# Optimization experiments

Measured on AMD Instinct MI355X. Metric: run time of the kernel, lower is better.

Reference implementation:

```python
import jax, jax.numpy as jnp
import numpy as np

U = 356  # LSTM units

def _lstm(x, W, Wr, b, h0, c0):
    """Keras-style LSTM. x: [B,T,F]. Returns (hs [B,T,U], h [B,U], c [B,U])."""
    def step(carry, xt):
        h, c = carry
        z = xt @ W + h @ Wr + b            # [B, 4U], gate order i,f,g,o
        i, f, g, o = jnp.split(z, 4, axis=-1)
        c = jax.nn.sigmoid(f) * c + jax.nn.sigmoid(i) * jnp.tanh(g)
        h = jax.nn.sigmoid(o) * jnp.tanh(c)
        return (h, c), h
    (h, c), hs = jax.lax.scan(step, (h0, c0), jnp.swapaxes(x, 0, 1))
    return jnp.swapaxes(hs, 0, 1), h, c


def setup_inputs() -> dict:
    key = jax.random.key(0)
    ks = jax.random.split(key, 12)
    s = 0.05
    return {
        "x": jax.random.normal(ks[0], (8192, 7, 69), jnp.float32),
        "m": jax.random.normal(ks[1], (8192, 7, 45), jnp.float32),
        "enc_W": jax.random.normal(ks[2], (69, 4 * U), jnp.float32) * s,
        "enc_U": jax.random.normal(ks[3], (U, 4 * U), jnp.float32) * s,
        "enc_b": jnp.zeros((4 * U,), jnp.float32),
        "dec_W": jax.random.normal(ks[4], (45, 4 * U), jnp.float32) * s,
        "dec_U": jax.random.normal(ks[5], (U, 4 * U), jnp.float32) * s,
        "dec_b": jnp.zeros((4 * U,), jnp.float32),
        "W_map": jax.random.normal(ks[6], (7 * U, 1024), jnp.float32) * s,
        "b_map": jnp.zeros((1024,), jnp.float32),
        "W1": jax.random.normal(ks[7], (1024, 1024), jnp.float32) * s,
        "b1": jnp.zeros((1024,), jnp.float32),
        "W2": jax.random.normal(ks[8], (1024, 1024), jnp.float32) * s,
        "b2": jnp.zeros((1024,), jnp.float32),
        "W3": jax.random.normal(ks[9], (1024, 1024), jnp.float32) * s,
        "b3": jnp.zeros((1024,), jnp.float32),
        "W_out": jax.random.normal(ks[10], (1024, 168), jnp.float32) * s,
        "b_out": jnp.zeros((168,), jnp.float32),
    }


def reference(x, m, enc_W, enc_U, enc_b, dec_W, dec_U, dec_b,
              W_map, b_map, W1, b1, W2, b2, W3, b3, W_out, b_out):
    B = x.shape[0]
    h0 = jnp.zeros((B, U), x.dtype)
    c0 = jnp.zeros((B, U), x.dtype)
    # Encoder: only final states are used (dropout layers are identity at inference).
    _, s_h, s_c = _lstm(x, enc_W, enc_U, enc_b, h0, c0)
    # Decoder seeded with encoder states, returns full sequence [B,7,U].
    decoded, _, _ = _lstm(m, dec_W, dec_U, dec_b, s_h, s_c)
    f = decoded.reshape(B, -1)                     # [B, 7*356]
    h = jax.nn.relu(f @ W_map + b_map)
    h = jnp.tanh(h @ W1 + b1)
    h = jnp.tanh(h @ W2 + b2)
    h = jnp.tanh(h @ W3 + b3)
    return h @ W_out + b_out                        # [B, 168]
```

## Files before the change

kernel.cpp:

```cpp
#include <hip/hip_runtime.h>
#include <math.h>


using bf16x8 = __attribute__((ext_vector_type(8))) short;
using f32x4  = __attribute__((ext_vector_type(4))) float;

enum { EPI_NONE = 0, EPI_RELU = 1, EPI_TANH = 2 };

__device__ inline unsigned short f2bf(float f) {
    union { float f; unsigned u; } v; v.f = f;
    unsigned r = v.u + 0x7FFFu + ((v.u >> 16) & 1u);
    return (unsigned short)(r >> 16);
}
__device__ inline float sigf(float x) {
    return __fdividef(1.f, 1.f + __expf(-x));
}
__device__ inline float tanhfast(float x) {
    return 1.f - __fdividef(2.f, 1.f + __expf(2.f * x));
}

__device__ inline void gll16(const void* g, void* l) {
    __builtin_amdgcn_global_load_lds(
        (const __attribute__((address_space(1))) unsigned int*)(uintptr_t)g,
        (__attribute__((address_space(3))) unsigned int*)(unsigned int)(uintptr_t)l,
        16, 0, 0);
}

#define PROWS 32
#define PLDA  456

#define STAGE_CHUNK(bufv, kkv, partv)                                          \
    _Pragma("unroll")                                                          \
    for (int q = 0; q < 4; ++q)                                                \
        gll16(Wt + (size_t)(kkv) * 49152 + (w * 12 + (partv) * 4 + q) * 512    \
                  + lane * 8,                                                  \
              (void*)&Bs[((w * 3 + (bufv)) * 4 + q) * 512 + lane * 8]);

#define LOADB4(dst, bufv)                                                      \
    _Pragma("unroll")                                                          \
    for (int q = 0; q < 4; ++q)                                                \
        dst[q] = *(const bf16x8*)&Bs[((w * 3 + (bufv)) * 4 + q) * 512          \
                                     + lane * 8];

#define LOADA(dst, kkv)                                                        \
    _Pragma("unroll")                                                          \
    for (int mi = 0; mi < 2; ++mi)                                             \
        dst[mi] = *(const bf16x8*)&Ab[(mi * 16 + lm) * PLDA + (kkv) * 32       \
                                      + quad * 8];

#define MFMA8(partv, bRv)                                                      \
    _Pragma("unroll")                                                          \
    for (int q = 0; q < 4; ++q) {                                              \
        acc[0][(partv) * 4 + q] = __builtin_amdgcn_mfma_f32_16x16x32_bf16(     \
            aF[0], bRv[q], acc[0][(partv) * 4 + q], 0, 0, 0);                  \
        acc[1][(partv) * 4 + q] = __builtin_amdgcn_mfma_f32_16x16x32_bf16(     \
            aF[1], bRv[q], acc[1][(partv) * 4 + q], 0, 0, 0);                  \
    }

#define VMWAIT(n)                                                              \
    asm volatile("s_waitcnt vmcnt(" #n ")" ::: "memory");                      \
    __builtin_amdgcn_sched_barrier(0);

__global__ __attribute__((amdgpu_flat_work_group_size(512, 512),
                          amdgpu_waves_per_eu(2, 2)))
void lstm_persist(const float* __restrict__ x,
                  const float* __restrict__ m,
                  const unsigned short* __restrict__ WtE,
                  const unsigned short* __restrict__ WtD,
                  const float* __restrict__ bIE,
                  const float* __restrict__ bID,
                  unsigned short* __restrict__ dcd)
{
    __shared__ __attribute__((aligned(16))) unsigned short Ab[PROWS * PLDA];
    __shared__ __attribute__((aligned(16))) unsigned short Bs[49152];
    const int tid  = threadIdx.x;
    const int lane = tid & 63;
    const int w    = tid >> 6;
    const int lm   = lane & 15, quad = lane >> 4;
    const int brow = blockIdx.x * PROWS;
    const int kk0  = blockIdx.x % 14;

    for (int i = tid; i < PROWS * PLDA; i += 512) Ab[i] = 0;
    __syncthreads();
    for (int i = tid; i < PROWS * 69; i += 512) {
        const int r = i / 69, f = i - r * 69;
        Ab[r * PLDA + f] = f2bf(x[((size_t)(brow + r) * 7 + 0) * 69 + f]);
    }

    float creg[2][3][4] = {};
    float bI[3][4];

    for (int s = 0; s < 14; ++s) {
        const bool enc = (s < 7);
        const int t = enc ? s : s - 7;
        const unsigned short* Wt = enc ? WtE : WtD;

        if (s == 0 || s == 7) {
            const float* bsrc = enc ? bIE : bID;
            #pragma unroll
            for (int a = 0; a < 3; ++a)
                #pragma unroll
                for (int g = 0; g < 4; ++g)
                    bI[a][g] = bsrc[(3 * w + a) * 64 + g * 16 + lm];
        }

        __syncthreads();

        f32x4 acc[2][12] = {};
        {
            STAGE_CHUNK(0, kk0, 0)
            STAGE_CHUNK(1, kk0, 1)
            int kkc = kk0;
            #pragma unroll 1
            for (int i = 0; i < 14; ++i) {
                const int kkn = (kkc == 13) ? 0 : kkc + 1;
                bf16x8 aF[2], bR[4];
                STAGE_CHUNK(2, kkc, 2)
                VMWAIT(8)
                LOADA(aF, kkc)
                LOADB4(bR, 0)
                MFMA8(0, bR)
                if (i < 13) {
                    STAGE_CHUNK(0, kkn, 0)
                    VMWAIT(8)
                } else {
                    VMWAIT(4)
                }
                LOADB4(bR, 1)
                MFMA8(1, bR)
                if (i < 13) {
                    STAGE_CHUNK(1, kkn, 1)
                    VMWAIT(8)
                } else {
                    VMWAIT(0)
                }
                LOADB4(bR, 2)
                MFMA8(2, bR)
                kkc = kkn;
            }
        }

        __syncthreads();

        const int hoff = (s < 6) ? 69 : 45;
        #pragma unroll
        for (int mi = 0; mi < 2; ++mi)
            #pragma unroll
            for (int a = 0; a < 3; ++a) {
                const int u = (3 * w + a) * 16 + lm;
                const bool uok = (u < 356);
                #pragma unroll
                for (int r = 0; r < 4; ++r) {
                    const float zi = acc[mi][a * 4 + 0][r] + bI[a][0];
                    const float zf = acc[mi][a * 4 + 1][r] + bI[a][1];
                    const float zg = acc[mi][a * 4 + 2][r] + bI[a][2];
                    const float zo = acc[mi][a * 4 + 3][r] + bI[a][3];
                    const float cn = sigf(zf) * creg[mi][a][r]
                                   + sigf(zi) * tanhfast(zg);
                    creg[mi][a][r] = cn;
                    const unsigned short hb = f2bf(sigf(zo) * tanhfast(cn));
                    const int rl = mi * 16 + quad * 4 + r;
                    if (uok) {
                        if (s < 13) Ab[rl * PLDA + hoff + u] = hb;
                        if (!enc)
                            dcd[(size_t)(brow + rl) * 2496 + t * 356 + u] = hb;
                    }
                }
            }

        const int sn = s + 1;
        if (sn < 7) {
            for (int i = tid; i < PROWS * 69; i += 512) {
                const int r = i / 69, f = i - r * 69;
                Ab[r * PLDA + f] =
                    f2bf(x[((size_t)(brow + r) * 7 + sn) * 69 + f]);
            }
        } else if (sn < 14) {
            for (int i = tid; i < PROWS * 45; i += 512) {
                const int r = i / 45, f = i - r * 45;
                Ab[r * PLDA + f] =
                    f2bf(m[((size_t)(brow + r) * 7 + (sn - 7)) * 45 + f]);
            }
        }
    }
}


#define STAGE(A_, Bt_, K_, k0_, b_)                                            \
    {                                                                          \
        const int row = tid >> 2, kc = tid & 3;                                \
        gll16((A_)  + (size_t)(m0 + row) * (K_) + (k0_) + kc * 8,              \
              (void*)&As[b_][tid * 8]);                                        \
        gll16((Bt_) + (size_t)(n0 + row) * (K_) + (k0_) + kc * 8,              \
              (void*)&Bs[b_][tid * 8]);                                        \
    }

#define GEMM_CORE(A_, Bt_, K_)                                                 \
    STAGE(A_, Bt_, K_, 0, 0)                                                   \
    {                                                                          \
        const int niter = (K_) / 32;                                           \
        for (int it = 0; it < niter; ++it) {                                   \
            __syncthreads();                                                   \
            if (it + 1 < niter) {                                              \
                const int kn = (it + 1) * 32, bn = (it + 1) & 1;               \
                STAGE(A_, Bt_, K_, kn, bn)                                     \
            }                                                                  \
            const unsigned short* Asb = As[it & 1];                            \
            const unsigned short* Bsb = Bs[it & 1];                            \
            bf16x8 aF[2], bF[4];                                               \
            _Pragma("unroll")                                                  \
            for (int mi = 0; mi < 2; ++mi)                                     \
                aF[mi] = *(const bf16x8*)(Asb + (wr*32 + mi*16 + lm)*32 + quad*8);\
            _Pragma("unroll")                                                  \
            for (int ni = 0; ni < 4; ++ni)                                     \
                bF[ni] = *(const bf16x8*)(Bsb + (wc*64 + ni*16 + lm)*32 + quad*8);\
            _Pragma("unroll")                                                  \
            for (int mi = 0; mi < 2; ++mi)                                     \
                _Pragma("unroll")                                              \
                for (int ni = 0; ni < 4; ++ni)                                 \
                    acc[mi][ni] = __builtin_amdgcn_mfma_f32_16x16x32_bf16(     \
                        aF[mi], bF[ni], acc[mi][ni], 0, 0, 0);                 \
        }                                                                      \
    }

#define GEMM_PREAMBLE                                                          \
    __shared__ __attribute__((aligned(16))) unsigned short As[2][128 * 32];    \
    __shared__ __attribute__((aligned(16))) unsigned short Bs[2][128 * 32];    \
    const int tid  = threadIdx.x;                                              \
    const int lane = tid & 63;                                                 \
    const int w    = tid >> 6;                                       \
    const int wr   = w >> 1, wc = w & 1;                    \
    const int lm   = lane & 15, quad = lane >> 4;                              \
    const int m0   = blockIdx.x * 128, n0 = blockIdx.y * 128;                  \
    f32x4 acc[2][4] = {};

template <int EPI, int OUT_BF16, int NGUARD>
__global__ __launch_bounds__(512, 6)
void gemm_mfma(const unsigned short* __restrict__ A,
               const unsigned short* __restrict__ Bt,
               const float* __restrict__ bias,
               void* __restrict__ Cv, int ldc, int Nreal, int K)
{
    GEMM_PREAMBLE
    GEMM_CORE(A, Bt, K)
    #pragma unroll
    for (int mi = 0; mi < 2; ++mi)
        #pragma unroll
        for (int r = 0; r < 4; ++r) {
            const size_t row = m0 + wr * 32 + mi * 16 + quad * 4 + r;
            #pragma unroll
            for (int ni = 0; ni < 4; ++ni) {
                const int col = n0 + wc * 64 + ni * 16 + lm;
                if (!NGUARD || col < Nreal) {
                    float v = acc[mi][ni][r] + bias[col];
                    if (EPI == EPI_RELU) v = fmaxf(v, 0.f);
                    if (EPI == EPI_TANH) v = tanhfast(v);
                    if (OUT_BF16) ((unsigned short*)Cv)[row * ldc + col] = f2bf(v);
                    else          ((float*)Cv)[row * ldc + col] = v;
                }
            }
        }
}

struct PackArgs {
    const float *Wa0, *Wb0, *bias0; unsigned short* Wt0; float* bI0; int K10, K0, Kp0;
    const float *Wa1, *Wb1, *bias1; unsigned short* Wt1; float* bI1; int K11, K1, Kp1;
};
__global__ void pack_lstm2(PackArgs p)
{
    const float* Wa  = blockIdx.y ? p.Wa1  : p.Wa0;
    const float* Wb  = blockIdx.y ? p.Wb1  : p.Wb0;
    const float* bias= blockIdx.y ? p.bias1: p.bias0;
    unsigned short* Wt = blockIdx.y ? p.Wt1 : p.Wt0;
    float* biasI = blockIdx.y ? p.bI1 : p.bI0;
    const int K1 = blockIdx.y ? p.K11 : p.K10;
    const int K  = blockIdx.y ? p.K1  : p.K0;
    const int Kp = blockIdx.y ? p.Kp1 : p.Kp0;
    const int idx = blockIdx.x * 256 + threadIdx.x;
    if (idx >= 1536 * Kp) return;
    const int np = idx / Kp, k = idx - np * Kp;
    const int ub = np >> 6, g = (np >> 4) & 3, ul = np & 15;
    const int u = ub * 16 + ul;
    const bool valid = (u < 356);
    const int norig = g * 356 + u;
    float v = 0.f;
    if (valid && k < K)
        v = (k < K1) ? Wa[(size_t)k * 1424 + norig]
                     : Wb[(size_t)(k - K1) * 1424 + norig];
    const int wv = np / 192, rem = np - wv * 192;
    const int ni = rem >> 4, lmv = rem & 15;
    const int kkv = k >> 5, kq = k & 31;
    const int qd = kq >> 3, j = kq & 7;
    Wt[(size_t)kkv * 49152 + (size_t)(wv * 12 + ni) * 512 + (qd * 16 + lmv) * 8 + j]
        = f2bf(v);
    if (k == 0) biasI[np] = valid ? bias[norig] : 0.f;
}

__global__ void transpose_pack(const float* __restrict__ W, int K, int N,
                               unsigned short* __restrict__ Wt, int Kp, int Np)
{
    __shared__ float t[32][33];
    const int n0 = blockIdx.x * 32, k0 = blockIdx.y * 32;
    const int tx = threadIdx.x, ty = threadIdx.y;
    #pragma unroll
    for (int r = 0; r < 4; ++r) {
        const int k = k0 + ty + 8 * r, n = n0 + tx;
        t[ty + 8 * r][tx] = (k < K && n < N) ? W[(size_t)k * N + n] : 0.f;
    }
    __syncthreads();
    #pragma unroll
    for (int r = 0; r < 4; ++r) {
        const int k = k0 + tx, n = n0 + ty + 8 * r;
        if (k < Kp && n < Np) Wt[(size_t)n * Kp + k] = f2bf(t[tx][ty + 8 * r]);
    }
}

struct WP3 { const float *s0, *s1, *s2; unsigned short *d0, *d1, *d2; };
__global__ void transpose_pack3(WP3 p)
{
    __shared__ float t[32][33];
    const float* W = (blockIdx.z == 0) ? p.s0 : (blockIdx.z == 1) ? p.s1 : p.s2;
    unsigned short* Wt = (blockIdx.z == 0) ? p.d0 : (blockIdx.z == 1) ? p.d1 : p.d2;
    const int n0 = blockIdx.x * 32, k0 = blockIdx.y * 32;
    const int tx = threadIdx.x, ty = threadIdx.y;
    #pragma unroll
    for (int r = 0; r < 4; ++r)
        t[ty + 8 * r][tx] = W[(size_t)(k0 + ty + 8 * r) * 1024 + n0 + tx];
    __syncthreads();
    #pragma unroll
    for (int r = 0; r < 4; ++r)
        Wt[(size_t)(n0 + ty + 8 * r) * 1024 + k0 + tx] = f2bf(t[tx][ty + 8 * r]);
}

__global__ void zero_dcd_pad(unsigned short* __restrict__ dcd)
{
    const int i = blockIdx.x * 256 + threadIdx.x;
    if (i < 8192 * 4) dcd[(size_t)(i >> 2) * 2496 + 2492 + (i & 3)] = 0;
}

extern "C" void kernel_launch(void* const* d_in, const int* in_sizes, int n_in,
                              void* d_out, int out_size, void* d_ws, size_t ws_size,
                              hipStream_t stream)
{
    const float* x     = (const float*)d_in[0];
    const float* m     = (const float*)d_in[1];
    const float* enc_W = (const float*)d_in[2];
    const float* enc_U = (const float*)d_in[3];
    const float* enc_b = (const float*)d_in[4];
    const float* dec_W = (const float*)d_in[5];
    const float* dec_Um= (const float*)d_in[6];
    const float* dec_b = (const float*)d_in[7];
    const float* W_map = (const float*)d_in[8];
    const float* b_map = (const float*)d_in[9];
    const float* W1    = (const float*)d_in[10];
    const float* b1    = (const float*)d_in[11];
    const float* W2    = (const float*)d_in[12];
    const float* b2    = (const float*)d_in[13];
    const float* W3    = (const float*)d_in[14];
    const float* b3    = (const float*)d_in[15];
    const float* W_out = (const float*)d_in[16];
    const float* b_out = (const float*)d_in[17];
    float* out = (float*)d_out;

    const int B = 8192, FE = 69, FD = 45;
    const int KMP = 2496;

    char* ws = (char*)d_ws;
    size_t off = 0;
    auto alloc = [&](size_t bytes) -> void* {
        void* p = ws + off; off = (off + bytes + 255) & ~(size_t)255; return p;
    };
    unsigned short* WtE = (unsigned short*)alloc((size_t)1536 * 448 * 2);
    unsigned short* WtD = (unsigned short*)alloc((size_t)1536 * 448 * 2);
    unsigned short* WtM = (unsigned short*)alloc((size_t)1024 * KMP * 2);
    unsigned short* Wt1 = (unsigned short*)alloc((size_t)1024 * 1024 * 2);
    unsigned short* Wt2 = (unsigned short*)alloc((size_t)1024 * 1024 * 2);
    unsigned short* Wt3 = (unsigned short*)alloc((size_t)1024 * 1024 * 2);
    unsigned short* WtO = (unsigned short*)alloc((size_t)256 * 1024 * 2);
    float* bIE = (float*)alloc(1536 * 4);
    float* bID = (float*)alloc(1536 * 4);
    unsigned short* dcd = (unsigned short*)alloc((size_t)B * KMP * 2);
    unsigned short* a1  = (unsigned short*)alloc((size_t)B * 1024 * 2);
    unsigned short* a2  = (unsigned short*)alloc((size_t)B * 1024 * 2);

    PackArgs pa{enc_W, enc_U, enc_b, WtE, bIE, FE, FE + 356, 448,
                dec_W, dec_Um, dec_b, WtD, bID, FD, FD + 356, 448};
    pack_lstm2<<<dim3((1536 * 448 + 255) / 256, 2), 256, 0, stream>>>(pa);
    const dim3 tb(32, 8);
    transpose_pack<<<dim3(1024 / 32, KMP / 32), tb, 0, stream>>>(
        W_map, 2492, 1024, WtM, KMP, 1024);
    WP3 p3{W1, W2, W3, Wt1, Wt2, Wt3};
    transpose_pack3<<<dim3(32, 32, 3), tb, 0, stream>>>(p3);
    transpose_pack<<<dim3(256 / 32, 1024 / 32), tb, 0, stream>>>(
        W_out, 1024, 168, WtO, 1024, 256);
    zero_dcd_pad<<<(8192 * 4 + 255) / 256, 256, 0, stream>>>(dcd);

    lstm_persist<<<256, 512, 0, stream>>>(x, m, WtE, WtD, bIE, bID, dcd);

    gemm_mfma<EPI_RELU, 1, 0><<<dim3(64, 8), 512, 0, stream>>>(
        dcd, WtM, b_map, a1, 1024, 1024, KMP);
    gemm_mfma<EPI_TANH, 1, 0><<<dim3(64, 8), 512, 0, stream>>>(
        a1, Wt1, b1, a2, 1024, 1024, 1024);
    gemm_mfma<EPI_TANH, 1, 0><<<dim3(64, 8), 512, 0, stream>>>(
        a2, Wt2, b2, a1, 1024, 1024, 1024);
    gemm_mfma<EPI_TANH, 1, 0><<<dim3(64, 8), 512, 0, stream>>>(
        a1, Wt3, b3, a2, 1024, 1024, 1024);
    gemm_mfma<EPI_NONE, 0, 1><<<dim3(64, 2), 512, 0, stream>>>(
        a2, WtO, b_out, out, 168, 168, 1024);
}
```

Baseline: 570.2 us.

## Split LSTM gate columns across 12 waves instead of 8 in persistent kernel

The persistent LSTM kernel now launches 768 threads per block (12 waves), and each wave owns 2 unit groups (8 gate tiles) instead of 3 (12 tiles). The weight staging pipeline shrinks from three chunk buffers per wave to two, with adjusted vmcnt waits, and the accumulator and cell-state register arrays get smaller. The aim is more waves sharing the recurrent GEMM per block, with less register pressure per wave, which should improve latency hiding. In exchange each wave issues fewer MFMAs between waits, so the shallower double-buffer may expose more load latency. The waves_per_eu hint is also removed.

```diff
diff --git a/kernel.cpp b/kernel.cpp
--- a/kernel.cpp
+++ b/kernel.cpp
@@ -32,14 +32,14 @@
 #define STAGE_CHUNK(bufv, kkv, partv)                                          \
     _Pragma("unroll")                                                          \
     for (int q = 0; q < 4; ++q)                                                \
-        gll16(Wt + (size_t)(kkv) * 49152 + (w * 12 + (partv) * 4 + q) * 512    \
+        gll16(Wt + (size_t)(kkv) * 49152 + (w * 8 + (partv) * 4 + q) * 512     \
                   + lane * 8,                                                  \
-              (void*)&Bs[((w * 3 + (bufv)) * 4 + q) * 512 + lane * 8]);
+              (void*)&Bs[((w * 2 + (bufv)) * 4 + q) * 512 + lane * 8]);
 
 #define LOADB4(dst, bufv)                                                      \
     _Pragma("unroll")                                                          \
     for (int q = 0; q < 4; ++q)                                                \
-        dst[q] = *(const bf16x8*)&Bs[((w * 3 + (bufv)) * 4 + q) * 512          \
+        dst[q] = *(const bf16x8*)&Bs[((w * 2 + (bufv)) * 4 + q) * 512          \
                                      + lane * 8];
 
 #define LOADA(dst, kkv)                                                        \
@@ -61,8 +61,7 @@
     asm volatile("s_waitcnt vmcnt(" #n ")" ::: "memory");                      \
     __builtin_amdgcn_sched_barrier(0);
 
-__global__ __attribute__((amdgpu_flat_work_group_size(512, 512),
-                          amdgpu_waves_per_eu(2, 2)))
+__global__ __attribute__((amdgpu_flat_work_group_size(768, 768)))
 void lstm_persist(const float* __restrict__ x,
                   const float* __restrict__ m,
                   const unsigned short* __restrict__ WtE,
@@ -80,15 +79,15 @@
     const int brow = blockIdx.x * PROWS;
     const int kk0  = blockIdx.x % 14;
 
-    for (int i = tid; i < PROWS * PLDA; i += 512) Ab[i] = 0;
+    for (int i = tid; i < PROWS * PLDA; i += 768) Ab[i] = 0;
     __syncthreads();
-    for (int i = tid; i < PROWS * 69; i += 512) {
+    for (int i = tid; i < PROWS * 69; i += 768) {
         const int r = i / 69, f = i - r * 69;
         Ab[r * PLDA + f] = f2bf(x[((size_t)(brow + r) * 7 + 0) * 69 + f]);
     }
 
-    float creg[2][3][4] = {};
-    float bI[3][4];
+    float creg[2][2][4] = {};
+    float bI[2][4];
 
     for (int s = 0; s < 14; ++s) {
         const bool enc = (s < 7);
@@ -98,15 +97,15 @@
         if (s == 0 || s == 7) {
             const float* bsrc = enc ? bIE : bID;
             #pragma unroll
-            for (int a = 0; a < 3; ++a)
+            for (int uu = 0; uu < 2; ++uu)
                 #pragma unroll
                 for (int g = 0; g < 4; ++g)
-                    bI[a][g] = bsrc[(3 * w + a) * 64 + g * 16 + lm];
+                    bI[uu][g] = bsrc[(2 * w + uu) * 64 + g * 16 + lm];
         }
 
         __syncthreads();
 
-        f32x4 acc[2][12] = {};
+        f32x4 acc[2][8] = {};
         {
             STAGE_CHUNK(0, kk0, 0)
             STAGE_CHUNK(1, kk0, 1)
@@ -115,27 +114,19 @@
             for (int i = 0; i < 14; ++i) {
                 const int kkn = (kkc == 13) ? 0 : kkc + 1;
                 bf16x8 aF[2], bR[4];
-                STAGE_CHUNK(2, kkc, 2)
-                VMWAIT(8)
+                VMWAIT(4)
                 LOADA(aF, kkc)
                 LOADB4(bR, 0)
                 MFMA8(0, bR)
+                if (i < 13) STAGE_CHUNK(0, kkn, 0)
                 if (i < 13) {
-                    STAGE_CHUNK(0, kkn, 0)
-                    VMWAIT(8)
+                    VMWAIT(4)
                 } else {
-                    VMWAIT(4)
+                    VMWAIT(0)
                 }
                 LOADB4(bR, 1)
                 MFMA8(1, bR)
-                if (i < 13) {
-                    STAGE_CHUNK(1, kkn, 1)
-                    VMWAIT(8)
-                } else {
-                    VMWAIT(0)
-                }
-                LOADB4(bR, 2)
-                MFMA8(2, bR)
+                if (i < 13) STAGE_CHUNK(1, kkn, 1)
                 kkc = kkn;
             }
         }
@@ -146,18 +137,18 @@
         #pragma unroll
         for (int mi = 0; mi < 2; ++mi)
             #pragma unroll
-            for (int a = 0; a < 3; ++a) {
-                const int u = (3 * w + a) * 16 + lm;
+            for (int uu = 0; uu < 2; ++uu) {
+                const int u = (2 * w + uu) * 16 + lm;
                 const bool uok = (u < 356);
                 #pragma unroll
                 for (int r = 0; r < 4; ++r) {
-                    const float zi = acc[mi][a * 4 + 0][r] + bI[a][0];
-                    const float zf = acc[mi][a * 4 + 1][r] + bI[a][1];
-                    const float zg = acc[mi][a * 4 + 2][r] + bI[a][2];
-                    const float zo = acc[mi][a * 4 + 3][r] + bI[a][3];
-                    const float cn = sigf(zf) * creg[mi][a][r]
+                    const float zi = acc[mi][uu * 4 + 0][r] + bI[uu][0];
+                    const float zf = acc[mi][uu * 4 + 1][r] + bI[uu][1];
+                    const float zg = acc[mi][uu * 4 + 2][r] + bI[uu][2];
+                    const float zo = acc[mi][uu * 4 + 3][r] + bI[uu][3];
+                    const float cn = sigf(zf) * creg[mi][uu][r]
                                    + sigf(zi) * tanhfast(zg);
-                    creg[mi][a][r] = cn;
+                    creg[mi][uu][r] = cn;
                     const unsigned short hb = f2bf(sigf(zo) * tanhfast(cn));
                     const int rl = mi * 16 + quad * 4 + r;
                     if (uok) {
@@ -170,13 +161,13 @@
 
         const int sn = s + 1;
         if (sn < 7) {
-            for (int i = tid; i < PROWS * 69; i += 512) {
+            for (int i = tid; i < PROWS * 69; i += 768) {
                 const int r = i / 69, f = i - r * 69;
                 Ab[r * PLDA + f] =
                     f2bf(x[((size_t)(brow + r) * 7 + sn) * 69 + f]);
             }
         } else if (sn < 14) {
-            for (int i = tid; i < PROWS * 45; i += 512) {
+            for (int i = tid; i < PROWS * 45; i += 768) {
                 const int r = i / 45, f = i - r * 45;
                 Ab[r * PLDA + f] =
                     f2bf(m[((size_t)(brow + r) * 7 + (sn - 7)) * 45 + f]);
@@ -395,7 +386,7 @@
         W_out, 1024, 168, WtO, 1024, 256);
     zero_dcd_pad<<<(8192 * 4 + 255) / 256, 256, 0, stream>>>(dcd);
 
-    lstm_persist<<<256, 512, 0, stream>>>(x, m, WtE, WtD, bIE, bID, dcd);
+    lstm_persist<<<256, 768, 0, stream>>>(x, m, WtE, WtD, bIE, bID, dcd);
 
     gemm_mfma<EPI_RELU, 1, 0><<<dim3(64, 8), 512, 0, stream>>>(
         dcd, WtM, b_map, a1, 1024, 1024, KMP);
```

Result: faster. 554.8 us (-2.7%).
